# Performance work log

Hardware: AMD Instinct MI355X
Metric: run time of the kernel (lower is better)

Reference implementation:

```python
import jax, jax.numpy as jnp
import numpy as np

K = 6  # knn_number
EPS_CS = 1e-8  # F.cosine_similarity eps


def _sqdist(a, b):
    # a: [B,N,3], b: [B,M,3] -> [B,N,M] squared euclidean distances
    return (jnp.sum(a * a, -1)[:, :, None]
            + jnp.sum(b * b, -1)[:, None, :]
            - 2.0 * jnp.einsum('bnc,bmc->bnm', a, b))


def _batch_norm(x):
    # normalize last dim with the module's exact epsilons
    n = jnp.sqrt(jnp.sum(x * x, axis=-1, keepdims=True) + 1e-08)
    return x / (n + 1e-10)


def _cossim(a, b):
    # torch F.cosine_similarity semantics along last dim
    na = jnp.maximum(jnp.sqrt(jnp.sum(a * a, -1)), EPS_CS)
    nb = jnp.maximum(jnp.sqrt(jnp.sum(b * b, -1)), EPS_CS)
    return jnp.sum(a * b, -1) / (na * nb)


def _gather(points, idx):
    # points: [B,N,C], idx: [B,...] int -> [B,...,C]
    return jax.vmap(lambda p, i: p[i])(points, idx)


def _avg_ori(group_ori, group_nor, batch_ori, batch_nor):
    # group_*: [B,N,K,3], batch_*: [B,N,3]
    nor_diff = jnp.sum(group_nor * batch_nor[:, :, None, :], axis=3)  # [B,N,K]
    nor_diff = jnp.exp(-nor_diff / 0.3) * 10.0 + 1.0
    nor_diff = jnp.where(nor_diff < 4.0, 1.0, 5.0)
    batch_ori_rot = jnp.cross(batch_ori, batch_nor)  # get_ori_rot90: ori x nor
    cos0 = _cossim(group_ori, batch_ori[:, :, None, :])       # [B,N,K]
    cos1 = _cossim(group_ori, batch_ori_rot[:, :, None, :])   # [B,N,K]
    cos = jnp.minimum(1.0 - jnp.abs(cos0), 1.0 - jnp.abs(cos1))
    return jnp.mean(nor_diff * cos)


def _forward(ori_pre, nor_pre, xyz_up, xyz_offset, pts, gt):
    ori_pre = _batch_norm(ori_pre)
    nor_pre = _batch_norm(nor_pre)
    xyz_gt = gt[:, :, 0:3]
    xyz_nor = gt[:, :, 3:6]

    # ori-loss: NN of pts in gt, gather gt normals
    index = jnp.argmin(_sqdist(pts, xyz_gt), axis=2)  # [B,N]
    nor_gt = _gather(xyz_nor, index)                  # [B,N,3]
    d_n = jnp.sum(nor_gt * ori_pre, axis=2, keepdims=True)
    ori_pro = _batch_norm(ori_pre - nor_gt * d_n)

    # smooth field over KNN (self-knn over pts, includes self)
    idx = jax.lax.top_k(-_sqdist(pts, pts), K)[1]  # [B,N,K]
    group_ori = _gather(ori_pro, idx)              # [B,N,K,3]
    group_nor = _gather(nor_gt, idx)
    loss_smooth = _avg_ori(group_ori, group_nor, ori_pro, nor_gt)

    # normal estimation loss
    loss_nor = jnp.mean(1.0 - jnp.abs(_cossim(nor_gt, nor_pre)))

    # chamfer distances (squared-dist chamfer)
    do = _sqdist(xyz_offset, xyz_gt)
    loss_charm_offset = jnp.mean(jnp.min(do, axis=2)) + jnp.mean(jnp.min(do, axis=1))
    du = _sqdist(xyz_up, xyz_gt)
    loss_charm = jnp.mean(jnp.min(du, axis=2)) + jnp.mean(jnp.min(du, axis=1))

    # nor-ori orthogonality
    loss_nor_ori = jnp.mean(jnp.abs(jnp.sum(ori_pre * nor_gt, axis=2)))

    loss_cd = loss_charm + 0.4 * loss_charm_offset
    loss = loss_smooth + loss_nor + 0.1 * loss_nor_ori + 200.0 * loss_cd
    return (loss, loss_smooth, loss_nor, loss_charm_offset, loss_nor_ori, loss_charm, loss_charm)


def setup_inputs() -> dict:
    key = jax.random.key(0)
    k = jax.random.split(key, 6)
    B, N, NG, NU = 4, 4096, 4096, 8192
    gt_xyz = jax.random.normal(k[5], (B, NG, 3), dtype=jnp.float32)
    gt_nor = _batch_norm(jax.random.normal(jax.random.fold_in(key, 7), (B, NG, 3), dtype=jnp.float32))
    return {
        'ori_pre': jax.random.normal(k[0], (B, N, 3), dtype=jnp.float32),
        'nor_pre': jax.random.normal(k[1], (B, N, 3), dtype=jnp.float32),
        'xyz_up': jax.random.normal(k[2], (B, NU, 3), dtype=jnp.float32),
        'xyz_offset': jax.random.normal(k[3], (B, NU, 3), dtype=jnp.float32),
        'pts': jax.random.normal(k[4], (B, N, 3), dtype=jnp.float32),
        'gt': jnp.concatenate([gt_xyz, gt_nor], axis=-1),
        'epoch': 1,
    }


def reference(ori_pre, nor_pre, xyz_up, xyz_offset, pts, gt, epoch):
    # epoch is unused by the original forward as well
    return _forward(ori_pre, nor_pre, xyz_up, xyz_offset, pts, gt)
```

## Files before the change

### kernel.cpp

```cpp
#include <hip/hip_runtime.h>
#include <stdint.h>

#define NN 4096
#define NGG 4096
#define NUU 8192

__device__ __forceinline__ unsigned fkey32(float f) {
  unsigned u = __float_as_uint(f);
  return u ^ (((int)u >> 31) | 0x80000000u);
}
__device__ __forceinline__ float unfkey32(unsigned k) {
  unsigned m = (k & 0x80000000u) ? 0x80000000u : 0xFFFFFFFFu;
  return __uint_as_float(k ^ m);
}

__device__ __forceinline__ float block_sum_256(float v, float* sbuf) {
#pragma unroll
  for (int o = 32; o > 0; o >>= 1) v += __shfl_down(v, o, 64);
  int lane = threadIdx.x & 63;
  int w = threadIdx.x >> 6;
  if (lane == 0) sbuf[w] = v;
  __syncthreads();
  float r = 0.f;
  if (threadIdx.x == 0) r = sbuf[0] + sbuf[1] + sbuf[2] + sbuf[3];
  __syncthreads();
  return r;
}

__device__ __forceinline__ float block_sum_512(float v, float* sbuf) {
#pragma unroll
  for (int o = 32; o > 0; o >>= 1) v += __shfl_down(v, o, 64);
  int lane = threadIdx.x & 63;
  int w = threadIdx.x >> 6;
  if (lane == 0) sbuf[w] = v;
  __syncthreads();
  float r = 0.f;
  if (threadIdx.x == 0) {
#pragma unroll
    for (int i = 0; i < 8; ++i) r += sbuf[i];
  }
  __syncthreads();
  return r;
}

__global__ __launch_bounds__(256) void k_scan(const float* __restrict__ pts,
                                              const float* __restrict__ gt,
                                              const float* __restrict__ up,
                                              const float* __restrict__ off,
                                              unsigned long long* __restrict__ keys,
                                              unsigned* __restrict__ rowmin,
                                              unsigned* __restrict__ colmin,
                                              float* __restrict__ acc) {
  __shared__ float4 sc[512];
  int blk = blockIdx.x;
  int tid = threadIdx.x;
  if (blk == 0 && tid < 16) acc[tid] = 0.f;

  if (blk < 512) {
    int qb = blk >> 3;
    int seg = blk & 7;
    int wb = qb >> 3;
    int which = wb >> 2;
    int b = wb & 3;
    int r0 = (qb & 7) * 1024 + tid * 4;
    {
      const float* gtb = gt + (size_t)b * NGG * 6 + (size_t)seg * 512 * 6;
      int i0 = tid * 2;
      const float4* g4 = (const float4*)(gtb + (size_t)i0 * 6);
      float4 u0 = g4[0], u1 = g4[1], u2 = g4[2];
      sc[i0] = make_float4(u0.x, u0.y, u0.z,
                           fmaf(u0.x, u0.x, fmaf(u0.y, u0.y, u0.z * u0.z)));
      sc[i0 + 1] = make_float4(u1.z, u1.w, u2.x,
                               fmaf(u1.z, u1.z, fmaf(u1.w, u1.w, u2.x * u2.x)));
    }
    const float* src = which ? up : off;
    const float4* s4 = (const float4*)src;
    size_t fb = ((size_t)(b * NUU + r0) * 3) >> 2;
    float4 A = s4[fb], B = s4[fb + 1], C = s4[fb + 2];
    float q0x = A.x, q0y = A.y, q0z = A.z;
    float q1x = A.w, q1y = B.x, q1z = B.y;
    float q2x = B.z, q2y = B.w, q2z = C.x;
    float q3x = C.y, q3y = C.z, q3z = C.w;
    float qq0 = fmaf(q0x, q0x, fmaf(q0y, q0y, q0z * q0z));
    float qq1 = fmaf(q1x, q1x, fmaf(q1y, q1y, q1z * q1z));
    float qq2 = fmaf(q2x, q2x, fmaf(q2y, q2y, q2z * q2z));
    float qq3 = fmaf(q3x, q3x, fmaf(q3y, q3y, q3z * q3z));
    float a0x = -2.f * q0x, a0y = -2.f * q0y, a0z = -2.f * q0z;
    float a1x = -2.f * q1x, a1y = -2.f * q1y, a1z = -2.f * q1z;
    float a2x = -2.f * q2x, a2y = -2.f * q2y, a2z = -2.f * q2z;
    float a3x = -2.f * q3x, a3y = -2.f * q3y, a3z = -2.f * q3z;
    __syncthreads();
    float b0 = 3.4e38f, b1 = 3.4e38f, b2 = 3.4e38f, b3 = 3.4e38f;
#pragma unroll 4
    for (int j = 0; j < 512; ++j) {
      float4 c = sc[j];
      float t;
      t = fmaf(c.x, a0x, c.w); t = fmaf(c.y, a0y, t); t = fmaf(c.z, a0z, t); b0 = fminf(b0, t);
      t = fmaf(c.x, a1x, c.w); t = fmaf(c.y, a1y, t); t = fmaf(c.z, a1z, t); b1 = fminf(b1, t);
      t = fmaf(c.x, a2x, c.w); t = fmaf(c.y, a2y, t); t = fmaf(c.z, a2z, t); b2 = fminf(b2, t);
      t = fmaf(c.x, a3x, c.w); t = fmaf(c.y, a3y, t); t = fmaf(c.z, a3z, t); b3 = fminf(b3, t);
    }
    int gr = which * 32768 + b * NUU + r0;
    atomicMin(&rowmin[gr + 0], fkey32(b0 + qq0));
    atomicMin(&rowmin[gr + 1], fkey32(b1 + qq1));
    atomicMin(&rowmin[gr + 2], fkey32(b2 + qq2));
    atomicMin(&rowmin[gr + 3], fkey32(b3 + qq3));

  } else if (blk < 1024) {
    int blk2 = blk - 512;
    int qb = blk2 >> 4;
    int seg = blk2 & 15;
    int which = qb >> 4;
    int b = (qb >> 2) & 3;
    int m0 = (qb & 3) * 1024 + tid * 4;
    const float* src = which ? up : off;
    if (tid < 128) {
      const float* sb = src + (size_t)b * NUU * 3 + (size_t)seg * 512 * 3;
      int i0 = tid * 4;
      const float4* s4 = (const float4*)(sb + (size_t)i0 * 3);
      float4 u0 = s4[0], u1 = s4[1], u2 = s4[2];
      sc[i0] = make_float4(u0.x, u0.y, u0.z,
                           fmaf(u0.x, u0.x, fmaf(u0.y, u0.y, u0.z * u0.z)));
      sc[i0 + 1] = make_float4(u0.w, u1.x, u1.y,
                               fmaf(u0.w, u0.w, fmaf(u1.x, u1.x, u1.y * u1.y)));
      sc[i0 + 2] = make_float4(u1.z, u1.w, u2.x,
                               fmaf(u1.z, u1.z, fmaf(u1.w, u1.w, u2.x * u2.x)));
      sc[i0 + 3] = make_float4(u2.y, u2.z, u2.w,
                               fmaf(u2.y, u2.y, fmaf(u2.z, u2.z, u2.w * u2.w)));
    }
    const float* g = gt + (size_t)b * NGG * 6 + (size_t)m0 * 6;
    float q0x = g[0],  q0y = g[1],  q0z = g[2];
    float q1x = g[6],  q1y = g[7],  q1z = g[8];
    float q2x = g[12], q2y = g[13], q2z = g[14];
    float q3x = g[18], q3y = g[19], q3z = g[20];
    float qq0 = fmaf(q0x, q0x, fmaf(q0y, q0y, q0z * q0z));
    float qq1 = fmaf(q1x, q1x, fmaf(q1y, q1y, q1z * q1z));
    float qq2 = fmaf(q2x, q2x, fmaf(q2y, q2y, q2z * q2z));
    float qq3 = fmaf(q3x, q3x, fmaf(q3y, q3y, q3z * q3z));
    float a0x = -2.f * q0x, a0y = -2.f * q0y, a0z = -2.f * q0z;
    float a1x = -2.f * q1x, a1y = -2.f * q1y, a1z = -2.f * q1z;
    float a2x = -2.f * q2x, a2y = -2.f * q2y, a2z = -2.f * q2z;
    float a3x = -2.f * q3x, a3y = -2.f * q3y, a3z = -2.f * q3z;
    __syncthreads();
    float b0 = 3.4e38f, b1 = 3.4e38f, b2 = 3.4e38f, b3 = 3.4e38f;
#pragma unroll 4
    for (int j = 0; j < 512; ++j) {
      float4 c = sc[j];
      float t;
      t = fmaf(c.x, a0x, c.w); t = fmaf(c.y, a0y, t); t = fmaf(c.z, a0z, t); b0 = fminf(b0, t);
      t = fmaf(c.x, a1x, c.w); t = fmaf(c.y, a1y, t); t = fmaf(c.z, a1z, t); b1 = fminf(b1, t);
      t = fmaf(c.x, a2x, c.w); t = fmaf(c.y, a2y, t); t = fmaf(c.z, a2z, t); b2 = fminf(b2, t);
      t = fmaf(c.x, a3x, c.w); t = fmaf(c.y, a3y, t); t = fmaf(c.z, a3z, t); b3 = fminf(b3, t);
    }
    int gc = which * 16384 + b * NGG + m0;
    atomicMin(&colmin[gc + 0], fkey32(b0 + qq0));
    atomicMin(&colmin[gc + 1], fkey32(b1 + qq1));
    atomicMin(&colmin[gc + 2], fkey32(b2 + qq2));
    atomicMin(&colmin[gc + 3], fkey32(b3 + qq3));

  } else {
    int blk3 = blk - 1024;
    int qb = blk3 >> 4;
    int seg = blk3 & 15;
    int b = qb >> 2;
    int m0 = (qb & 3) * 1024 + tid * 4;
    if (tid < 128) {
      const float* gtb = gt + (size_t)b * NGG * 6 + (size_t)seg * 256 * 6;
      int i0 = tid * 2;
      const float4* g4 = (const float4*)(gtb + (size_t)i0 * 6);
      float4 u0 = g4[0], u1 = g4[1], u2 = g4[2];
      sc[i0] = make_float4(u0.x, u0.y, u0.z,
                           fmaf(u0.x, u0.x, fmaf(u0.y, u0.y, u0.z * u0.z)));
      sc[i0 + 1] = make_float4(u1.z, u1.w, u2.x,
                               fmaf(u1.z, u1.z, fmaf(u1.w, u1.w, u2.x * u2.x)));
    }
    size_t fb = ((size_t)(b * NN + m0) * 3) >> 2;
    const float4* p4 = (const float4*)pts;
    float4 A = p4[fb], B = p4[fb + 1], C = p4[fb + 2];
    float q0x = A.x, q0y = A.y, q0z = A.z;
    float q1x = A.w, q1y = B.x, q1z = B.y;
    float q2x = B.z, q2y = B.w, q2z = C.x;
    float q3x = C.y, q3y = C.z, q3z = C.w;
    float a0x = -2.f * q0x, a0y = -2.f * q0y, a0z = -2.f * q0z;
    float a1x = -2.f * q1x, a1y = -2.f * q1y, a1z = -2.f * q1z;
    float a2x = -2.f * q2x, a2y = -2.f * q2y, a2z = -2.f * q2z;
    float a3x = -2.f * q3x, a3y = -2.f * q3y, a3z = -2.f * q3z;
    __syncthreads();
    float b0 = 3.4e38f, b1 = 3.4e38f, b2 = 3.4e38f, b3 = 3.4e38f;
    int i0 = 0, i1 = 0, i2 = 0, i3 = 0;
#pragma unroll 4
    for (int j = 0; j < 256; ++j) {
      float4 c = sc[j];
      float t; bool cc;
      t = fmaf(c.x, a0x, c.w); t = fmaf(c.y, a0y, t); t = fmaf(c.z, a0z, t);
      cc = t < b0; b0 = cc ? t : b0; i0 = cc ? j : i0;
      t = fmaf(c.x, a1x, c.w); t = fmaf(c.y, a1y, t); t = fmaf(c.z, a1z, t);
      cc = t < b1; b1 = cc ? t : b1; i1 = cc ? j : i1;
      t = fmaf(c.x, a2x, c.w); t = fmaf(c.y, a2y, t); t = fmaf(c.z, a2z, t);
      cc = t < b2; b2 = cc ? t : b2; i2 = cc ? j : i2;
      t = fmaf(c.x, a3x, c.w); t = fmaf(c.y, a3y, t); t = fmaf(c.z, a3z, t);
      cc = t < b3; b3 = cc ? t : b3; i3 = cc ? j : i3;
    }
    int q = b * NN + m0;
    int base = seg * 256;
    atomicMin(&keys[q + 0], ((unsigned long long)fkey32(b0) << 32) | (unsigned)(base + i0));
    atomicMin(&keys[q + 1], ((unsigned long long)fkey32(b1) << 32) | (unsigned)(base + i1));
    atomicMin(&keys[q + 2], ((unsigned long long)fkey32(b2) << 32) | (unsigned)(base + i2));
    atomicMin(&keys[q + 3], ((unsigned long long)fkey32(b3) << 32) | (unsigned)(base + i3));
  }
}

__global__ __launch_bounds__(256) void k_post(
    const float* __restrict__ ori_pre, const float* __restrict__ nor_pre,
    const float* __restrict__ gt, const unsigned long long* __restrict__ keys,
    const unsigned* __restrict__ rowmin, const unsigned* __restrict__ colmin,
    float* __restrict__ nor_gt, float* __restrict__ ori_pro, float* __restrict__ acc) {
  __shared__ float sb1[4], sb2[4];
  int blk = blockIdx.x;
  if (blk < 64) {
    int q = blk * 256 + threadIdx.x;
    int b = q >> 12;
    float ox = ori_pre[q * 3 + 0], oy = ori_pre[q * 3 + 1], oz = ori_pre[q * 3 + 2];
    float n1 = sqrtf(fmaf(ox, ox, fmaf(oy, oy, oz * oz)) + 1e-8f) + 1e-10f;
    ox /= n1; oy /= n1; oz /= n1;
    float px = nor_pre[q * 3 + 0], py = nor_pre[q * 3 + 1], pz = nor_pre[q * 3 + 2];
    float n2 = sqrtf(fmaf(px, px, fmaf(py, py, pz * pz)) + 1e-8f) + 1e-10f;
    px /= n2; py /= n2; pz /= n2;
    unsigned idx = (unsigned)(keys[q] & 0xffffffffULL);
    const float* g = gt + (size_t)b * NGG * 6 + (size_t)idx * 6 + 3;
    float gx = g[0], gy = g[1], gz = g[2];
    float dn = fmaf(gx, ox, fmaf(gy, oy, gz * oz));
    float vx = ox - gx * dn, vy = oy - gy * dn, vz = oz - gz * dn;
    float n3 = sqrtf(fmaf(vx, vx, fmaf(vy, vy, vz * vz)) + 1e-8f) + 1e-10f;
    vx /= n3; vy /= n3; vz /= n3;
    nor_gt[q * 3 + 0] = gx; nor_gt[q * 3 + 1] = gy; nor_gt[q * 3 + 2] = gz;
    ori_pro[q * 3 + 0] = vx; ori_pro[q * 3 + 1] = vy; ori_pro[q * 3 + 2] = vz;
    float na = fmaxf(sqrtf(fmaf(gx, gx, fmaf(gy, gy, gz * gz))), 1e-8f);
    float nb = fmaxf(sqrtf(fmaf(px, px, fmaf(py, py, pz * pz))), 1e-8f);
    float cs = fmaf(gx, px, fmaf(gy, py, gz * pz)) / (na * nb);
    float t_nor = 1.f - fabsf(cs);
    float t_ori = fabsf(dn);
    float s1 = block_sum_256(t_nor, sb1);
    float s2 = block_sum_256(t_ori, sb2);
    if (threadIdx.x == 0) {
      atomicAdd(&acc[1], s1);
      atomicAdd(&acc[2], s2);
    }
  } else {
    int rblk = blk - 64;
    float v;
    int slot;
    if (rblk < 256) {
      int i = rblk * 256 + threadIdx.x;
      v = unfkey32(rowmin[i]);
      slot = (i >> 15) ? 5 : 3;
    } else {
      int i = (rblk - 256) * 256 + threadIdx.x;
      v = unfkey32(colmin[i]);
      slot = (i >> 14) ? 6 : 4;
    }
    float s = block_sum_256(v, sb1);
    if (threadIdx.x == 0) atomicAdd(&acc[slot], s);
  }
}

__global__ __launch_bounds__(512) void k_knn_smooth(const float* __restrict__ pts,
                                                    const float* __restrict__ nor_gt,
                                                    const float* __restrict__ ori_pro,
                                                    float* __restrict__ acc,
                                                    float* __restrict__ out) {
  __shared__ float4 sp[1152];
  __shared__ float sbuf[8];
  int tid = threadIdx.x;
  int q_local = tid >> 5;
  int t = tid & 31;
  int q = blockIdx.x * 16 + q_local;
  int b = q >> 12;
  int n = q & 4095;
  const float* pb = pts + (size_t)b * NN * 3;
  float qx = pb[n * 3 + 0], qy = pb[n * 3 + 1], qz = pb[n * 3 + 2];
  float qx2 = -2.f * qx, qy2 = -2.f * qy, qz2 = -2.f * qz;
  float d0 = 3.4e38f, d1 = 3.4e38f, d2 = 3.4e38f,
        d3 = 3.4e38f, d4 = 3.4e38f, d5 = 3.4e38f;
  int i0 = 0, i1 = 0, i2 = 0, i3 = 0, i4 = 0, i5 = 0;

  for (int ch = 0; ch < 4; ++ch) {
    if (tid < 256) {
      const float4* p4 = (const float4*)(pb + (size_t)(ch * 1024 + tid * 4) * 3);
      float4 u0 = p4[0], u1 = p4[1], u2 = p4[2];
      int il = tid * 4;
      int si = il + (il >> 3);
      sp[si] = make_float4(u0.x, u0.y, u0.z,
                           fmaf(u0.x, u0.x, fmaf(u0.y, u0.y, u0.z * u0.z)));
      sp[si + 1] = make_float4(u0.w, u1.x, u1.y,
                               fmaf(u0.w, u0.w, fmaf(u1.x, u1.x, u1.y * u1.y)));
      sp[si + 2] = make_float4(u1.z, u1.w, u2.x,
                               fmaf(u1.z, u1.z, fmaf(u1.w, u1.w, u2.x * u2.x)));
      sp[si + 3] = make_float4(u2.y, u2.z, u2.w,
                               fmaf(u2.y, u2.y, fmaf(u2.z, u2.z, u2.w * u2.w)));
    }
    __syncthreads();
    int cbase = ch << 10;
    for (int jo = 0; jo < 4; ++jo) {
      float T = d5;
#pragma unroll
      for (int o = 16; o > 0; o >>= 1) T = fminf(T, __shfl_xor(T, o, 32));
#pragma unroll
      for (int ji = 0; ji < 8; ++ji) {
        int c = (((jo << 3) | ji) << 5) | t;
        float4 p = sp[c + (c >> 3)];
        float d = fmaf(p.x, qx2, p.w);
        d = fmaf(p.y, qy2, d);
        d = fmaf(p.z, qz2, d);
        if (d <= T) {
          int ci = cbase | c;
          bool cc; float nd; int ni;
          cc = d < d0; nd = cc ? d : d0; d = cc ? d0 : d; ni = cc ? ci : i0; ci = cc ? i0 : ci; d0 = nd; i0 = ni;
          cc = d < d1; nd = cc ? d : d1; d = cc ? d1 : d; ni = cc ? ci : i1; ci = cc ? i1 : ci; d1 = nd; i1 = ni;
          cc = d < d2; nd = cc ? d : d2; d = cc ? d2 : d; ni = cc ? ci : i2; ci = cc ? i2 : ci; d2 = nd; i2 = ni;
          cc = d < d3; nd = cc ? d : d3; d = cc ? d3 : d; ni = cc ? ci : i3; ci = cc ? i3 : ci; d3 = nd; i3 = ni;
          cc = d < d4; nd = cc ? d : d4; d = cc ? d4 : d; ni = cc ? ci : i4; ci = cc ? i4 : ci; d4 = nd; i4 = ni;
          cc = d < d5; nd = cc ? d : d5;                  ni = cc ? ci : i5;                    d5 = nd; i5 = ni;
        }
      }
    }
    __syncthreads();
  }

  int myid = 0;
#pragma unroll
  for (int r = 0; r < 6; ++r) {
    unsigned long long h = ((unsigned long long)fkey32(d0) << 32) | (unsigned)i0;
    unsigned long long m = h;
#pragma unroll
    for (int o = 16; o > 0; o >>= 1) {
      unsigned long long other = __shfl_xor(m, o, 32);
      m = (other < m) ? other : m;
    }
    if (t == r) myid = (int)(m & 0xffffffffULL);
    if (h == m) {
      d0 = d1; i0 = i1; d1 = d2; i1 = i2; d2 = d3; i2 = i3;
      d3 = d4; i3 = i4; d4 = d5; i4 = i5; d5 = 3.4e38f;
    }
  }

  float sum = 0.f;
  if (t < 6) {
    const float* gq = nor_gt + (size_t)q * 3;
    float ngx = gq[0], ngy = gq[1], ngz = gq[2];
    const float* oq = ori_pro + (size_t)q * 3;
    float box = oq[0], boy = oq[1], boz = oq[2];
    float rx = boy * ngz - boz * ngy;
    float ry = boz * ngx - box * ngz;
    float rz = box * ngy - boy * ngx;
    float nbo = fmaxf(sqrtf(fmaf(box, box, fmaf(boy, boy, boz * boz))), 1e-8f);
    float nrot = fmaxf(sqrtf(fmaf(rx, rx, fmaf(ry, ry, rz * rz))), 1e-8f);
    const float* gn = nor_gt + (size_t)(b * 4096 + myid) * 3;
    const float* go = ori_pro + (size_t)(b * 4096 + myid) * 3;
    float gnx = gn[0], gny = gn[1], gnz = gn[2];
    float gox = go[0], goy = go[1], goz = go[2];
    float ndv = fmaf(gnx, ngx, fmaf(gny, ngy, gnz * ngz));
    float wv = (expf(-ndv / 0.3f) * 10.f + 1.f) < 4.f ? 1.f : 5.f;
    float ngo = fmaxf(sqrtf(fmaf(gox, gox, fmaf(goy, goy, goz * goz))), 1e-8f);
    float c0 = fmaf(gox, box, fmaf(goy, boy, goz * boz)) / (ngo * nbo);
    float c1 = fmaf(gox, rx, fmaf(goy, ry, goz * rz)) / (ngo * nrot);
    float cosv = fminf(1.f - fabsf(c0), 1.f - fabsf(c1));
    sum = wv * cosv;
  }
  float s = block_sum_512(sum, sbuf);

  if (tid == 0) {
    atomicAdd(&acc[0], s);
    __threadfence();
    unsigned c = atomicAdd((unsigned*)(acc + 9), 1u);
    if (c == gridDim.x - 1) {
      __threadfence();
      float a0 = atomicAdd(&acc[0], 0.f);
      float a1 = atomicAdd(&acc[1], 0.f);
      float a2 = atomicAdd(&acc[2], 0.f);
      float a3 = atomicAdd(&acc[3], 0.f);
      float a4 = atomicAdd(&acc[4], 0.f);
      float a5 = atomicAdd(&acc[5], 0.f);
      float a6 = atomicAdd(&acc[6], 0.f);
      float loss_smooth = a0 / 98304.f;
      float loss_nor = a1 / 16384.f;
      float loss_nor_ori = a2 / 16384.f;
      float lco = a3 / 32768.f + a4 / 16384.f;
      float lc = a5 / 32768.f + a6 / 16384.f;
      float loss_cd = lc + 0.4f * lco;
      float loss = loss_smooth + loss_nor + 0.1f * loss_nor_ori + 200.f * loss_cd;
      out[0] = loss;
      out[1] = loss_smooth;
      out[2] = loss_nor;
      out[3] = lco;
      out[4] = loss_nor_ori;
      out[5] = lc;
      out[6] = lc;
    }
  }
}

extern "C" void kernel_launch(void* const* d_in, const int* in_sizes, int n_in,
                              void* d_out, int out_size, void* d_ws, size_t ws_size,
                              hipStream_t stream) {
  (void)in_sizes; (void)n_in; (void)out_size; (void)ws_size;
  const float* ori_pre = (const float*)d_in[0];
  const float* nor_pre = (const float*)d_in[1];
  const float* xyz_up = (const float*)d_in[2];
  const float* xyz_off = (const float*)d_in[3];
  const float* pts = (const float*)d_in[4];
  const float* gt = (const float*)d_in[5];
  float* out = (float*)d_out;
  char* ws = (char*)d_ws;

  float* acc = (float*)(ws + 0);
  unsigned long long* keys = (unsigned long long*)(ws + 512);
  unsigned* rowmin = (unsigned*)(ws + 512 + 131072);
  unsigned* colmin = (unsigned*)(ws + 512 + 131072 + 262144);
  float* nor_gt = (float*)(ws + 512 + 131072 + 262144 + 131072);
  float* ori_pro = (float*)(ws + 512 + 131072 + 262144 + 131072 + 196608);

  hipMemsetAsync(ws + 512, 0xFF, 131072 + 262144 + 131072, stream);

  k_scan<<<1280, 256, 0, stream>>>(pts, gt, xyz_up, xyz_off, keys, rowmin,
                                   colmin, acc);
  k_post<<<448, 256, 0, stream>>>(ori_pre, nor_pre, gt, keys, rowmin, colmin,
                                  nor_gt, ori_pro, acc);
  k_knn_smooth<<<1024, 512, 0, stream>>>(pts, nor_gt, ori_pro, acc, out);
}
```

Baseline: 198.5 us.

## Prune KNN candidates with per-wave minima threshold before top-6 selection

Rewrites the self-KNN smooth kernel. Each thread now holds 8 candidate points in registers and computes distances to the block's 16 queries. A per-query threshold is set to the 6th smallest of the 8 per-wave minima, which is a valid upper bound on the 6th nearest distance. Only candidates under that threshold are appended to a small shared survivor list, and a 3-deep per-lane list plus wave reductions then picks the final 6. This drops the old design's shared-memory staging of all points and its per-candidate insertion sort over 4096 points per query. The trade-off is that survivors are capped at 96 per query, so correctness depends on that bound not being exceeded.

```diff
diff --git a/kernel.cpp b/kernel.cpp
--- a/kernel.cpp
+++ b/kernel.cpp
@@ -264,84 +264,134 @@
   }
 }
 
-__global__ __launch_bounds__(512) void k_knn_smooth(const float* __restrict__ pts,
-                                                    const float* __restrict__ nor_gt,
-                                                    const float* __restrict__ ori_pro,
-                                                    float* __restrict__ acc,
-                                                    float* __restrict__ out) {
-  __shared__ float4 sp[1152];
-  __shared__ float sbuf[8];
+__global__ __launch_bounds__(512, 4) void k_knn_smooth(const float* __restrict__ pts,
+                                                       const float* __restrict__ nor_gt,
+                                                       const float* __restrict__ ori_pro,
+                                                       float* __restrict__ acc,
+                                                       float* __restrict__ out) {
+  __shared__ unsigned long long surv[16][96];
+  __shared__ unsigned scnt[16];
+  __shared__ float wmin[8][16];
+  __shared__ float stau[16];
+  __shared__ float sred[8];
   int tid = threadIdx.x;
+  int lane = tid & 63;
+  int wave = tid >> 6;
+  int blk = blockIdx.x;
+  int b = blk >> 8;
+  const float* pb = pts + (size_t)b * NN * 3;
+
+  if (tid < 16) scnt[tid] = 0;
+
+  const float* pq = pb + (size_t)((blk & 255) * 16) * 3;
+  float q2x[16], q2y[16], q2z[16];
+#pragma unroll
+  for (int qq = 0; qq < 16; ++qq) {
+    q2x[qq] = -2.f * pq[qq * 3 + 0];
+    q2y[qq] = -2.f * pq[qq * 3 + 1];
+    q2z[qq] = -2.f * pq[qq * 3 + 2];
+  }
+
+  float cx[8], cy[8], cz[8], cw[8];
+  {
+    const float4* p4 = (const float4*)(pb + (size_t)tid * 24);
+    float4 u0 = p4[0], u1 = p4[1], u2 = p4[2], u3 = p4[3], u4 = p4[4], u5 = p4[5];
+    cx[0] = u0.x; cy[0] = u0.y; cz[0] = u0.z;
+    cx[1] = u0.w; cy[1] = u1.x; cz[1] = u1.y;
+    cx[2] = u1.z; cy[2] = u1.w; cz[2] = u2.x;
+    cx[3] = u2.y; cy[3] = u2.z; cz[3] = u2.w;
+    cx[4] = u3.x; cy[4] = u3.y; cz[4] = u3.z;
+    cx[5] = u3.w; cy[5] = u4.x; cz[5] = u4.y;
+    cx[6] = u4.z; cy[6] = u4.w; cz[6] = u5.x;
+    cx[7] = u5.y; cy[7] = u5.z; cz[7] = u5.w;
+#pragma unroll
+    for (int c = 0; c < 8; ++c)
+      cw[c] = fmaf(cx[c], cx[c], fmaf(cy[c], cy[c], cz[c] * cz[c]));
+  }
+
+  float m[16];
+#pragma unroll
+  for (int qq = 0; qq < 16; ++qq) {
+    float mm = 3.4e38f;
+#pragma unroll
+    for (int c = 0; c < 8; ++c) {
+      float d = fmaf(cx[c], q2x[qq], cw[c]);
+      d = fmaf(cy[c], q2y[qq], d);
+      d = fmaf(cz[c], q2z[qq], d);
+      mm = fminf(mm, d);
+    }
+    m[qq] = mm;
+  }
+
+#pragma unroll
+  for (int qq = 0; qq < 16; ++qq) {
+    float w = m[qq];
+#pragma unroll
+    for (int o = 32; o > 0; o >>= 1) w = fminf(w, __shfl_xor(w, o, 64));
+    if (lane == 0) wmin[wave][qq] = w;
+  }
+  __syncthreads();
+
+  if (tid < 16) {
+    float vv[8];
+#pragma unroll
+    for (int i = 0; i < 8; ++i) vv[i] = wmin[i][tid];
+    float tau = 3.4e38f;
+#pragma unroll
+    for (int i = 0; i < 8; ++i) {
+      int cnt = 0;
+#pragma unroll
+      for (int j = 0; j < 8; ++j) cnt += (vv[j] <= vv[i]) ? 1 : 0;
+      if (cnt >= 6) tau = fminf(tau, vv[i]);
+    }
+    stau[tid] = tau;
+  }
+  __syncthreads();
+
+#pragma unroll
+  for (int qq = 0; qq < 16; ++qq) {
+    if (m[qq] <= stau[qq]) {
+      float tq = stau[qq];
+#pragma unroll
+      for (int c = 0; c < 8; ++c) {
+        float d = fmaf(cx[c], q2x[qq], cw[c]);
+        d = fmaf(cy[c], q2y[qq], d);
+        d = fmaf(cz[c], q2z[qq], d);
+        if (d <= tq) {
+          unsigned slot = atomicAdd(&scnt[qq], 1u);
+          if (slot < 96)
+            surv[qq][slot] =
+                ((unsigned long long)fkey32(d) << 32) | (unsigned)(tid * 8 + c);
+        }
+      }
+    }
+  }
+  __syncthreads();
+
   int q_local = tid >> 5;
   int t = tid & 31;
-  int q = blockIdx.x * 16 + q_local;
-  int b = q >> 12;
-  int n = q & 4095;
-  const float* pb = pts + (size_t)b * NN * 3;
-  float qx = pb[n * 3 + 0], qy = pb[n * 3 + 1], qz = pb[n * 3 + 2];
-  float qx2 = -2.f * qx, qy2 = -2.f * qy, qz2 = -2.f * qz;
-  float d0 = 3.4e38f, d1 = 3.4e38f, d2 = 3.4e38f,
-        d3 = 3.4e38f, d4 = 3.4e38f, d5 = 3.4e38f;
-  int i0 = 0, i1 = 0, i2 = 0, i3 = 0, i4 = 0, i5 = 0;
-
-  for (int ch = 0; ch < 4; ++ch) {
-    if (tid < 256) {
-      const float4* p4 = (const float4*)(pb + (size_t)(ch * 1024 + tid * 4) * 3);
-      float4 u0 = p4[0], u1 = p4[1], u2 = p4[2];
-      int il = tid * 4;
-      int si = il + (il >> 3);
-      sp[si] = make_float4(u0.x, u0.y, u0.z,
-                           fmaf(u0.x, u0.x, fmaf(u0.y, u0.y, u0.z * u0.z)));
-      sp[si + 1] = make_float4(u0.w, u1.x, u1.y,
-                               fmaf(u0.w, u0.w, fmaf(u1.x, u1.x, u1.y * u1.y)));
-      sp[si + 2] = make_float4(u1.z, u1.w, u2.x,
-                               fmaf(u1.z, u1.z, fmaf(u1.w, u1.w, u2.x * u2.x)));
-      sp[si + 3] = make_float4(u2.y, u2.z, u2.w,
-                               fmaf(u2.y, u2.y, fmaf(u2.z, u2.z, u2.w * u2.w)));
-    }
-    __syncthreads();
-    int cbase = ch << 10;
-    for (int jo = 0; jo < 4; ++jo) {
-      float T = d5;
-#pragma unroll
-      for (int o = 16; o > 0; o >>= 1) T = fminf(T, __shfl_xor(T, o, 32));
-#pragma unroll
-      for (int ji = 0; ji < 8; ++ji) {
-        int c = (((jo << 3) | ji) << 5) | t;
-        float4 p = sp[c + (c >> 3)];
-        float d = fmaf(p.x, qx2, p.w);
-        d = fmaf(p.y, qy2, d);
-        d = fmaf(p.z, qz2, d);
-        if (d <= T) {
-          int ci = cbase | c;
-          bool cc; float nd; int ni;
-          cc = d < d0; nd = cc ? d : d0; d = cc ? d0 : d; ni = cc ? ci : i0; ci = cc ? i0 : ci; d0 = nd; i0 = ni;
-          cc = d < d1; nd = cc ? d : d1; d = cc ? d1 : d; ni = cc ? ci : i1; ci = cc ? i1 : ci; d1 = nd; i1 = ni;
-          cc = d < d2; nd = cc ? d : d2; d = cc ? d2 : d; ni = cc ? ci : i2; ci = cc ? i2 : ci; d2 = nd; i2 = ni;
-          cc = d < d3; nd = cc ? d : d3; d = cc ? d3 : d; ni = cc ? ci : i3; ci = cc ? i3 : ci; d3 = nd; i3 = ni;
-          cc = d < d4; nd = cc ? d : d4; d = cc ? d4 : d; ni = cc ? ci : i4; ci = cc ? i4 : ci; d4 = nd; i4 = ni;
-          cc = d < d5; nd = cc ? d : d5;                  ni = cc ? ci : i5;                    d5 = nd; i5 = ni;
-        }
-      }
-    }
-    __syncthreads();
-  }
-
+  int q = blk * 16 + q_local;
+  unsigned cnt = scnt[q_local];
+  if (cnt > 96) cnt = 96;
+  unsigned long long l0 = ~0ULL, l1 = ~0ULL, l2 = ~0ULL;
+  for (int i = t; i < (int)cnt; i += 32) {
+    unsigned long long k = surv[q_local][i];
+    bool cc; unsigned long long nk;
+    cc = k < l0; nk = cc ? k : l0; k = cc ? l0 : k; l0 = nk;
+    cc = k < l1; nk = cc ? k : l1; k = cc ? l1 : k; l1 = nk;
+    cc = k < l2; nk = cc ? k : l2;                  l2 = nk;
+  }
   int myid = 0;
 #pragma unroll
   for (int r = 0; r < 6; ++r) {
-    unsigned long long h = ((unsigned long long)fkey32(d0) << 32) | (unsigned)i0;
-    unsigned long long m = h;
+    unsigned long long h = l0, mk = l0;
 #pragma unroll
     for (int o = 16; o > 0; o >>= 1) {
-      unsigned long long other = __shfl_xor(m, o, 32);
-      m = (other < m) ? other : m;
-    }
-    if (t == r) myid = (int)(m & 0xffffffffULL);
-    if (h == m) {
-      d0 = d1; i0 = i1; d1 = d2; i1 = i2; d2 = d3; i2 = i3;
-      d3 = d4; i3 = i4; d4 = d5; i4 = i5; d5 = 3.4e38f;
-    }
+      unsigned long long other = __shfl_xor(mk, o, 32);
+      mk = (other < mk) ? other : mk;
+    }
+    if (t == r) myid = (int)(mk & 0xffffffffULL);
+    if (h == mk) { l0 = l1; l1 = l2; l2 = ~0ULL; }
   }
 
   float sum = 0.f;
@@ -367,7 +417,7 @@
     float cosv = fminf(1.f - fabsf(c0), 1.f - fabsf(c1));
     sum = wv * cosv;
   }
-  float s = block_sum_512(sum, sbuf);
+  float s = block_sum_512(sum, sred);
 
   if (tid == 0) {
     atomicAdd(&acc[0], s);
```

Result: slower. 237.5 us (+19.7%).
